# Kernel tuning notes

Measured on AMD Instinct MI355X. Metric: run time of the kernel, lower is better.

## Reference

```python
import jax, jax.numpy as jnp
import numpy as np
import math

N, NCB, DIM, CB = 16384, 16, 4, 1024
LOG2 = math.log(2.0)


def setup_inputs() -> dict:
    key = jax.random.key(0)
    k1, k2, k3 = jax.random.split(key, 3)
    x = jax.random.normal(k1, (N, NCB, DIM), jnp.float32)
    # codebook init ~ N(0, 1/sqrt(cb_dim)) as in the torch module
    codebook = jax.random.normal(k2, (NCB, CB, DIM), jnp.float32) / math.sqrt(DIM)
    logits = 0.01 * jax.random.normal(k3, (NCB, CB), jnp.float32)
    lmbda = jnp.asarray(128.0, jnp.float32)
    return {"x": x, "codebook": codebook, "logits": logits, "lmbda": lmbda}


def reference(x, codebook, logits, lmbda):
    # Unconditional entropy model: log2 pmf from softmax over logits
    log2_pmf_u = jax.nn.log_softmax(logits, axis=-1) / (-LOG2)      # (ncb, cb)
    rate_bias = log2_pmf_u / lmbda                                   # (ncb, cb)

    # Squared L2 distance: (N, ncb, cb)
    dist = ((x * x).sum(-1)[..., None]
            + (codebook * codebook).sum(-1)[None]
            - 2.0 * jnp.einsum('nad,acd->nac', x, codebook))
    dist = dist + rate_bias[None]

    index = jnp.argmin(dist, axis=-1)                                # (N, ncb)
    cb_idx = jnp.arange(NCB)[None, :]                                # (1, ncb)

    # one-hot @ codebook == gather of selected codewords
    x_hat = codebook[cb_idx, index]                                  # (N, ncb, dim)
    # (one_hot * log2_pmf_u).sum() == sum of selected log2 probs
    rate_uem = log2_pmf_u[cb_idx, index].sum()

    rate_cem = jnp.zeros((), x.dtype)
    prior_dist = jnp.zeros((1,), x.dtype)
    param_bit = jnp.zeros((1,), x.dtype)
    return (x_hat, rate_uem, rate_cem, prior_dist, param_bit)
```

## Files before the change

kernel.cpp:

```cpp
#include <hip/hip_runtime.h>

#define N_ROWS 16384
#define NCB    16
#define CB     1024
#define TPB    256

__global__ void zero_tail_kernel(float* p) {
    int t = threadIdx.x;
    if (t < 4) p[t] = 0.0f;
}

__global__ __launch_bounds__(256) void prep_kernel(
    const float4* __restrict__ cbook,
    const float*  __restrict__ logits,
    const float*  __restrict__ lmbda_p,
    float* __restrict__ ws_cnb,
    float* __restrict__ ws_l2u)
{
    const int a = blockIdx.x;
    const int t = threadIdx.x;
    __shared__ float sredA[4], sredB[4];

    float l[4];
    float m = -INFINITY;
#pragma unroll
    for (int r = 0; r < 4; ++r) {
        l[r] = logits[a * CB + t + 256 * r];
        m = fmaxf(m, l[r]);
    }
#pragma unroll
    for (int off = 32; off >= 1; off >>= 1) m = fmaxf(m, __shfl_down(m, off, 64));
    if ((t & 63) == 0) sredA[t >> 6] = m;
    __syncthreads();
    const float gmax = fmaxf(fmaxf(sredA[0], sredA[1]), fmaxf(sredA[2], sredA[3]));

    float s = 0.f;
#pragma unroll
    for (int r = 0; r < 4; ++r) s += __expf(l[r] - gmax);
#pragma unroll
    for (int off = 32; off >= 1; off >>= 1) s += __shfl_down(s, off, 64);
    if ((t & 63) == 0) sredB[t >> 6] = s;
    __syncthreads();
    const float lse   = gmax + __logf(sredB[0] + sredB[1] + sredB[2] + sredB[3]);
    const float inv_l = 1.0f / lmbda_p[0];
    const float INV_LN2 = 1.4426950408889634f;
#pragma unroll
    for (int r = 0; r < 4; ++r) {
        int i = t + 256 * r;
        float4 w = cbook[a * CB + i];
        float v  = (lse - l[r]) * INV_LN2;
        ws_l2u[a * CB + i] = v;
        ws_cnb[a * CB + i] = w.x * w.x + w.y * w.y + w.z * w.z + w.w * w.w
                           + v * inv_l;
    }
}

__global__ __launch_bounds__(TPB) void ecvq_kernel(
    const float4* __restrict__ x,
    const float4* __restrict__ cbook,
    const float*  __restrict__ ws_cnb,
    const float*  __restrict__ ws_l2u,
    float4* __restrict__ xhat,
    float*  __restrict__ tail)
{
    __shared__ float4 s_cb[CB];
    __shared__ float  s_l2u[CB];

    const int a     = blockIdx.x;
    const int chunk = blockIdx.y;
    const int t     = threadIdx.x;

#pragma unroll
    for (int r = 0; r < CB / TPB; ++r) {
        int i = t + TPB * r;
        s_cb[i]  = cbook[a * CB + i];
        s_l2u[i] = ws_l2u[a * CB + i];
    }

    const int n = chunk * TPB + t;
    const float4 xv = x[n * NCB + a];
    const float4 xm2 = make_float4(-2.f * xv.x, -2.f * xv.y,
                                   -2.f * xv.z, -2.f * xv.w);
    __syncthreads();

    const float4* __restrict__ cb  = cbook  + a * CB;
    const float*  __restrict__ cnb = ws_cnb + a * CB;

    float dmin = INFINITY;
    int   imin = 0;
#pragma unroll 8
    for (int c = 0; c < CB; ++c) {
        const float4 w = cb[c];
        float d = xm2.x * w.x;
        d = fmaf(xm2.y, w.y, d);
        d = fmaf(xm2.z, w.z, d);
        d = fmaf(xm2.w, w.w, d);
        d += cnb[c];
        bool lt = d < dmin;
        dmin = lt ? d : dmin;
        imin = lt ? c : imin;
    }

    xhat[n * NCB + a] = s_cb[imin];
    float rsum = s_l2u[imin];
#pragma unroll
    for (int off = 32; off >= 1; off >>= 1) rsum += __shfl_down(rsum, off, 64);
    __shared__ float wsum[TPB / 64];
    if ((t & 63) == 0) wsum[t >> 6] = rsum;
    __syncthreads();
    if (t == 0) {
        float tot = wsum[0];
#pragma unroll
        for (int w = 1; w < TPB / 64; ++w) tot += wsum[w];
        atomicAdd(&tail[0], tot);
    }
}

extern "C" void kernel_launch(void* const* d_in, const int* in_sizes, int n_in,
                              void* d_out, int out_size, void* d_ws, size_t ws_size,
                              hipStream_t stream) {
    (void)in_sizes; (void)n_in; (void)out_size; (void)ws_size;
    const float4* x      = (const float4*)d_in[0];
    const float4* cbook  = (const float4*)d_in[1];
    const float*  logits = (const float*)d_in[2];
    const float*  lmbda  = (const float*)d_in[3];

    float* out  = (float*)d_out;
    float* tail = out + (size_t)N_ROWS * NCB * 4;

    float* ws_cnb = (float*)d_ws;
    float* ws_l2u = ws_cnb + NCB * CB;

    zero_tail_kernel<<<1, 64, 0, stream>>>(tail);
    prep_kernel<<<NCB, 256, 0, stream>>>(cbook, logits, lmbda, ws_cnb, ws_l2u);

    dim3 grid(NCB, N_ROWS / TPB);
    ecvq_kernel<<<grid, TPB, 0, stream>>>(x, cbook, ws_cnb, ws_l2u,
                                          (float4*)d_out, tail);
}
```

Before: 140.7 us.

## Split codebook search across two thread halves and drop shared-memory staging

Each block now handles 128 rows with two thread groups, each scanning half of the 1024 codewords, then merging the argmin through shared memory. The shared-memory copy of the codebook and log-probs is removed; the final gather reads global memory directly. It also folds the norm term into the first FMA and uses fminf for the running minimum. Total work stays the same but per-thread loop length halves, with grid blocks doubling and an extra sync/merge step added.

```diff
diff --git a/kernel.cpp b/kernel.cpp
--- a/kernel.cpp
+++ b/kernel.cpp
@@ -3,7 +3,8 @@
 #define N_ROWS 16384
 #define NCB    16
 #define CB     1024
-#define TPB    256
+#define HALF   512
+#define RPB    128
 
 __global__ void zero_tail_kernel(float* p) {
     int t = threadIdx.x;
@@ -55,7 +56,7 @@
     }
 }
 
-__global__ __launch_bounds__(TPB) void ecvq_kernel(
+__global__ __launch_bounds__(256) void ecvq_kernel(
     const float4* __restrict__ x,
     const float4* __restrict__ cbook,
     const float*  __restrict__ ws_cnb,
@@ -63,57 +64,53 @@
     float4* __restrict__ xhat,
     float*  __restrict__ tail)
 {
-    __shared__ float4 s_cb[CB];
-    __shared__ float  s_l2u[CB];
+    const int a  = blockIdx.x;
+    const int tx = threadIdx.x;
+    const int h  = threadIdx.y;
+    const int n  = blockIdx.y * RPB + tx;
 
-    const int a     = blockIdx.x;
-    const int chunk = blockIdx.y;
-    const int t     = threadIdx.x;
-
-#pragma unroll
-    for (int r = 0; r < CB / TPB; ++r) {
-        int i = t + TPB * r;
-        s_cb[i]  = cbook[a * CB + i];
-        s_l2u[i] = ws_l2u[a * CB + i];
-    }
-
-    const int n = chunk * TPB + t;
     const float4 xv = x[n * NCB + a];
     const float4 xm2 = make_float4(-2.f * xv.x, -2.f * xv.y,
                                    -2.f * xv.z, -2.f * xv.w);
-    __syncthreads();
 
-    const float4* __restrict__ cb  = cbook  + a * CB;
-    const float*  __restrict__ cnb = ws_cnb + a * CB;
+    const int cbase = h * HALF;
+    const float4* __restrict__ cb  = cbook  + a * CB + cbase;
+    const float*  __restrict__ cnb = ws_cnb + a * CB + cbase;
 
     float dmin = INFINITY;
-    int   imin = 0;
-#pragma unroll 8
-    for (int c = 0; c < CB; ++c) {
+    int   imin = cbase;
+#pragma unroll 16
+    for (int c = 0; c < HALF; ++c) {
         const float4 w = cb[c];
-        float d = xm2.x * w.x;
+        float d = fmaf(xm2.x, w.x, cnb[c]);
         d = fmaf(xm2.y, w.y, d);
         d = fmaf(xm2.z, w.z, d);
         d = fmaf(xm2.w, w.w, d);
-        d += cnb[c];
-        bool lt = d < dmin;
-        dmin = lt ? d : dmin;
-        imin = lt ? c : imin;
+        imin = (d < dmin) ? (cbase + c) : imin;
+        dmin = fminf(dmin, d);
     }
 
-    xhat[n * NCB + a] = s_cb[imin];
-    float rsum = s_l2u[imin];
+    __shared__ float s_d[RPB];
+    __shared__ int   s_i[RPB];
+    if (h == 1) { s_d[tx] = dmin; s_i[tx] = imin; }
+    __syncthreads();
+
+    float rsum = 0.f;
+    if (h == 0) {
+        float d1 = s_d[tx];
+        if (d1 < dmin) { dmin = d1; imin = s_i[tx]; }
+        xhat[n * NCB + a] = cbook[a * CB + imin];
+        rsum = ws_l2u[a * CB + imin];
+    }
+
 #pragma unroll
     for (int off = 32; off >= 1; off >>= 1) rsum += __shfl_down(rsum, off, 64);
-    __shared__ float wsum[TPB / 64];
-    if ((t & 63) == 0) wsum[t >> 6] = rsum;
+    __shared__ float wsum[4];
+    const int lin = tx + RPB * h;
+    if ((lin & 63) == 0) wsum[lin >> 6] = rsum;
     __syncthreads();
-    if (t == 0) {
-        float tot = wsum[0];
-#pragma unroll
-        for (int w = 1; w < TPB / 64; ++w) tot += wsum[w];
-        atomicAdd(&tail[0], tot);
-    }
+    if (lin == 0)
+        atomicAdd(&tail[0], wsum[0] + wsum[1] + wsum[2] + wsum[3]);
 }
 
 extern "C" void kernel_launch(void* const* d_in, const int* in_sizes, int n_in,
@@ -134,7 +131,8 @@
     zero_tail_kernel<<<1, 64, 0, stream>>>(tail);
     prep_kernel<<<NCB, 256, 0, stream>>>(cbook, logits, lmbda, ws_cnb, ws_l2u);
 
-    dim3 grid(NCB, N_ROWS / TPB);
-    ecvq_kernel<<<grid, TPB, 0, stream>>>(x, cbook, ws_cnb, ws_l2u,
-                                          (float4*)d_out, tail);
+    dim3 block(RPB, 2);
+    dim3 grid(NCB, N_ROWS / RPB);
+    ecvq_kernel<<<grid, block, 0, stream>>>(x, cbook, ws_cnb, ws_l2u,
+                                            (float4*)d_out, tail);
 }
```

Measured after the change: 212.1 us. +50.7%, slower.

## Interleave codebook with folded bias table and scan two rows per thread

Applied to the files above, without the earlier changes.

The prep kernel now writes an interleaved table holding each codeword and a precomputed bias -0.5*(||c||^2 + rate/lambda) plus its log2 prob. The scan maximises x·c + g instead of minimising the full distance, which drops the -2 scaling and the separate add. Each thread handles two rows, so every codeword load is reused twice, and the shared-memory staging is removed. The cost is half as many blocks, which reduces parallelism, and tie-breaking and rounding change slightly because of the algebraic rearrangement.

```diff
diff --git a/kernel.cpp b/kernel.cpp
--- a/kernel.cpp
+++ b/kernel.cpp
@@ -4,6 +4,8 @@
 #define NCB    16
 #define CB     1024
 #define TPB    256
+#define RPT    2
+#define RPB    (TPB * RPT)
 
 __global__ void zero_tail_kernel(float* p) {
     int t = threadIdx.x;
@@ -14,8 +16,7 @@
     const float4* __restrict__ cbook,
     const float*  __restrict__ logits,
     const float*  __restrict__ lmbda_p,
-    float* __restrict__ ws_cnb,
-    float* __restrict__ ws_l2u)
+    float4* __restrict__ tb)
 {
     const int a = blockIdx.x;
     const int t = threadIdx.x;
@@ -49,66 +50,60 @@
         int i = t + 256 * r;
         float4 w = cbook[a * CB + i];
         float v  = (lse - l[r]) * INV_LN2;
-        ws_l2u[a * CB + i] = v;
-        ws_cnb[a * CB + i] = w.x * w.x + w.y * w.y + w.z * w.z + w.w * w.w
-                           + v * inv_l;
+        float cc = w.x * w.x + w.y * w.y + w.z * w.z + w.w * w.w;
+        float g  = -0.5f * (cc + v * inv_l);
+        tb[(size_t)(a * CB + i) * 2]     = w;
+        tb[(size_t)(a * CB + i) * 2 + 1] = make_float4(g, v, 0.f, 0.f);
     }
 }
 
-__global__ __launch_bounds__(TPB) void ecvq_kernel(
+__global__ __launch_bounds__(TPB) void scan_kernel(
     const float4* __restrict__ x,
-    const float4* __restrict__ cbook,
-    const float*  __restrict__ ws_cnb,
-    const float*  __restrict__ ws_l2u,
+    const float4* __restrict__ tb,
     float4* __restrict__ xhat,
     float*  __restrict__ tail)
 {
-    __shared__ float4 s_cb[CB];
-    __shared__ float  s_l2u[CB];
-
     const int a     = blockIdx.x;
     const int chunk = blockIdx.y;
-    const int t     = threadIdx.x;
+    const int tx    = threadIdx.x;
+
+    const int n0 = chunk * RPB + tx;
+    const int n1 = n0 + TPB;
+    const float4 x0 = x[n0 * NCB + a];
+    const float4 x1 = x[n1 * NCB + a];
+
+    const float4* __restrict__ t = tb + (size_t)a * CB * 2;
+
+    float s0 = -INFINITY, s1 = -INFINITY;
+    int   i0 = 0,         i1 = 0;
+#pragma unroll 8
+    for (int c = 0; c < CB; ++c) {
+        const float4 w = t[2 * c];
+        const float  g = t[2 * c + 1].x;
+        float d0 = fmaf(x0.w, w.w, g);
+        d0 = fmaf(x0.z, w.z, d0);
+        d0 = fmaf(x0.y, w.y, d0);
+        d0 = fmaf(x0.x, w.x, d0);
+        float d1 = fmaf(x1.w, w.w, g);
+        d1 = fmaf(x1.z, w.z, d1);
+        d1 = fmaf(x1.y, w.y, d1);
+        d1 = fmaf(x1.x, w.x, d1);
+        i0 = (d0 > s0) ? c : i0;
+        s0 = fmaxf(s0, d0);
+        i1 = (d1 > s1) ? c : i1;
+        s1 = fmaxf(s1, d1);
+    }
+
+    xhat[n0 * NCB + a] = t[2 * i0];
+    xhat[n1 * NCB + a] = t[2 * i1];
+    float r = t[2 * i0 + 1].y + t[2 * i1 + 1].y;
 
 #pragma unroll
-    for (int r = 0; r < CB / TPB; ++r) {
-        int i = t + TPB * r;
-        s_cb[i]  = cbook[a * CB + i];
-        s_l2u[i] = ws_l2u[a * CB + i];
-    }
-
-    const int n = chunk * TPB + t;
-    const float4 xv = x[n * NCB + a];
-    const float4 xm2 = make_float4(-2.f * xv.x, -2.f * xv.y,
-                                   -2.f * xv.z, -2.f * xv.w);
+    for (int off = 32; off >= 1; off >>= 1) r += __shfl_down(r, off, 64);
+    __shared__ float wsum[TPB / 64];
+    if ((tx & 63) == 0) wsum[tx >> 6] = r;
     __syncthreads();
-
-    const float4* __restrict__ cb  = cbook  + a * CB;
-    const float*  __restrict__ cnb = ws_cnb + a * CB;
-
-    float dmin = INFINITY;
-    int   imin = 0;
-#pragma unroll 8
-    for (int c = 0; c < CB; ++c) {
-        const float4 w = cb[c];
-        float d = xm2.x * w.x;
-        d = fmaf(xm2.y, w.y, d);
-        d = fmaf(xm2.z, w.z, d);
-        d = fmaf(xm2.w, w.w, d);
-        d += cnb[c];
-        bool lt = d < dmin;
-        dmin = lt ? d : dmin;
-        imin = lt ? c : imin;
-    }
-
-    xhat[n * NCB + a] = s_cb[imin];
-    float rsum = s_l2u[imin];
-#pragma unroll
-    for (int off = 32; off >= 1; off >>= 1) rsum += __shfl_down(rsum, off, 64);
-    __shared__ float wsum[TPB / 64];
-    if ((t & 63) == 0) wsum[t >> 6] = rsum;
-    __syncthreads();
-    if (t == 0) {
+    if (tx == 0) {
         float tot = wsum[0];
 #pragma unroll
         for (int w = 1; w < TPB / 64; ++w) tot += wsum[w];
@@ -128,13 +123,11 @@
     float* out  = (float*)d_out;
     float* tail = out + (size_t)N_ROWS * NCB * 4;
 
-    float* ws_cnb = (float*)d_ws;
-    float* ws_l2u = ws_cnb + NCB * CB;
+    float4* tb = (float4*)d_ws;
 
     zero_tail_kernel<<<1, 64, 0, stream>>>(tail);
-    prep_kernel<<<NCB, 256, 0, stream>>>(cbook, logits, lmbda, ws_cnb, ws_l2u);
+    prep_kernel<<<NCB, 256, 0, stream>>>(cbook, logits, lmbda, tb);
 
-    dim3 grid(NCB, N_ROWS / TPB);
-    ecvq_kernel<<<grid, TPB, 0, stream>>>(x, cbook, ws_cnb, ws_l2u,
-                                          (float4*)d_out, tail);
+    dim3 grid(NCB, N_ROWS / RPB);
+    scan_kernel<<<grid, TPB, 0, stream>>>(x, tb, (float4*)d_out, tail);
 }
```

Measured after the change: 225.7 us. 1.6x slower.
